# Performance work log

Measured on AMD Instinct MI355X. Metric: run time of the kernel, lower is better.

Reference implementation:

```python
import jax, jax.numpy as jnp
import numpy as np

N_SIGMA = 2
N_CLASS = 8
FG_WEIGHT = jnp.array([10., 10., 10., 40., 80., 100., 60., 20.], dtype=jnp.float32)
W_INST, W_VAR, W_SEED = 1.0, 10.0, 1.0
MIN_PIXELS = 128


def lovasz_hinge_flat(logits, labels):
    # logits, labels: [P] flat; labels in {0,1}
    signs = 2.0 * labels - 1.0
    errors = 1.0 - logits * signs
    order = jnp.argsort(-errors)  # descending
    errors_sorted = errors[order]
    gt_sorted = labels[order]
    gts = gt_sorted.sum()
    inter = gts - jnp.cumsum(gt_sorted)
    union = gts + jnp.cumsum(1.0 - gt_sorted)
    jac = 1.0 - inter / union
    grad = jnp.concatenate([jac[:1], jac[1:] - jac[:-1]])
    return jnp.dot(jax.nn.relu(errors_sorted), jax.lax.stop_gradient(grad))


def setup_inputs() -> dict:
    key = jax.random.key(0)
    k1, k2, k3, k4 = jax.random.split(key, 4)
    B, H, W, N = 2, 512, 1024, 8
    prediction = jax.random.normal(k1, (B, 12, H, W), dtype=jnp.float32)
    bbox = jax.random.randint(k2, (B, 9, H, W), 0, 2, dtype=jnp.int32)
    masks = jax.random.randint(k3, (B, N, H, W), 0, 2, dtype=jnp.int32)
    cls_ids = jax.random.randint(k4, (B, N), 0, 8, dtype=jnp.int32)
    return {"prediction": prediction, "bbox": bbox, "masks": masks, "cls_ids": cls_ids}


def _forward(prediction, bbox, masks, cls_ids):
    B, C, H, W = prediction.shape
    N = masks.shape[1]
    sg = jax.lax.stop_gradient
    # coordinate map: full 2048/1024 linspace sliced to [:W]/[:H], as in the buffer
    xm = jnp.linspace(0.0, 2.0, 2048, dtype=prediction.dtype)[:W]
    ym = jnp.linspace(0.0, 1.0, 1024, dtype=prediction.dtype)[:H]
    xym = jnp.stack([jnp.broadcast_to(xm[None, :], (H, W)),
                     jnp.broadcast_to(ym[:, None], (H, W))], axis=0)  # [2,H,W]

    spatial_emb = jnp.tanh(prediction[:, 0:2]) + xym[None]            # [B,2,H,W]
    sigma = prediction[:, 2:2 + N_SIGMA]                               # [B,2,H,W]
    seed = jax.nn.sigmoid(prediction[:, 2 + N_SIGMA:2 + N_SIGMA + N_CLASS])  # [B,8,H,W]

    # background seed loss: sum over cls 1..8 of seed[cls-1]^2 where bbox[cls]==0
    bg = bbox[:, 1:9] == 0                                             # [B,8,H,W]
    seed_bg = jnp.sum(jnp.where(bg, seed * seed, 0.0), axis=(1, 2, 3))  # [B]

    m = (masks > 0).astype(prediction.dtype)                           # [B,N,H,W]
    cnt = m.sum(axis=(2, 3))                                           # [B,N]
    valid = (cnt >= MIN_PIXELS).astype(prediction.dtype)               # [B,N]
    cnt_safe = jnp.maximum(cnt, 1.0)

    # per-instance masked means (to_center=False -> center from spatial_emb)
    center = jnp.einsum('bnhw,bchw->bnc', m, spatial_emb) / cnt_safe[..., None]  # [B,N,2]
    s_mean = jnp.einsum('bnhw,bchw->bnc', m, sigma) / cnt_safe[..., None]        # [B,N,2]

    # var loss: mean over [n_sigma, P] of (sigma_in - s.detach())^2
    diff2 = (sigma[:, None] - sg(s_mean)[..., None, None]) ** 2        # [B,N,2,H,W]
    var_inst = jnp.einsum('bnchw,bnhw->bn', diff2, m) / (N_SIGMA * cnt_safe)

    s_exp = jnp.exp(s_mean * 10.0)                                     # [B,N,2]
    d2 = (spatial_emb[:, None] - center[..., None, None]) ** 2         # [B,N,2,H,W]
    dist = jnp.exp(-jnp.einsum('bnchw,bnc->bnhw', d2, s_exp))          # [B,N,H,W]

    # lovasz hinge per instance on dist*2-1 vs mask
    logits = (dist * 2.0 - 1.0).reshape(B * N, H * W)
    labels = m.reshape(B * N, H * W)
    lov = jax.vmap(lovasz_hinge_flat)(logits, labels).reshape(B, N)    # [B,N]

    # foreground seed loss
    seed_cls = jnp.take_along_axis(seed, cls_ids[..., None, None].astype(jnp.int32), axis=1)  # [B,N,H,W]
    fw = FG_WEIGHT[cls_ids]                                            # [B,N]
    seed_fg = fw * jnp.einsum('bnhw,bnhw->bn', m, (seed_cls - sg(dist)) ** 2)

    obj = valid.sum(axis=1)                                            # [B]
    obj_safe = jnp.maximum(obj, 1.0)
    inst_l = jnp.sum(lov * valid, axis=1) / obj_safe
    var_l = jnp.sum(var_inst * valid, axis=1) / obj_safe
    seed_l = (seed_bg + jnp.sum(seed_fg * valid, axis=1)) / (H * W)
    loss = jnp.mean(W_INST * inst_l + W_VAR * var_l + W_SEED * seed_l)
    return loss


def reference(prediction, bbox, masks, cls_ids):
    return _forward(prediction, bbox, masks, cls_ids)
```

## Files before the change

kernel.cpp:

```cpp
#include <hip/hip_runtime.h>
#include <cstdint>
#include <cstddef>

#define HW 524288
#define HW4 131072
#define NBIN 1024


__device__ __forceinline__ float wred(float v) {
#pragma unroll
  for (int o = 32; o > 0; o >>= 1) v += __shfl_xor(v, o, 64);
  return v;
}

__device__ __forceinline__ float fsig(float x) {
  return __builtin_amdgcn_rcpf(1.f + __expf(-x));
}
__device__ __forceinline__ float ftanh(float x) {
  return 1.f - 2.f * __builtin_amdgcn_rcpf(__expf(2.f * x) + 1.f);
}

__global__ __launch_bounds__(256) void pass1(
    const float* __restrict__ pred, const int* __restrict__ masks,
    double* __restrict__ acc)
{
  const int b = blockIdx.y;
  const int tid = threadIdx.x;
  const float4* pb4 = (const float4*)(pred + (size_t)b * 12 * HW);
  const int4*   mk4 = (const int4*)(masks + (size_t)b * 8 * HW);

  float c[8] = {0}, cx[8] = {0}, cy[8] = {0}, sx[8] = {0}, sy[8] = {0},
        sxx[8] = {0}, syy[8] = {0};

#pragma unroll
  for (int k = 0; k < 2; k++) {
    const int g = blockIdx.x * 512 + k * 256 + tid;
    int idx = g << 2;
    int h = idx >> 10, w = idx & 1023;
    float4 p0 = pb4[g];
    float4 p1 = pb4[HW4 + g];
    float4 s0 = pb4[2 * HW4 + g];
    float4 s1 = pb4[3 * HW4 + g];
    int4 mv[8];
#pragma unroll
    for (int n = 0; n < 8; n++) mv[n] = mk4[n * HW4 + g];

    float p0v[4] = {p0.x, p0.y, p0.z, p0.w}, p1v[4] = {p1.x, p1.y, p1.z, p1.w};
    float s0v[4] = {s0.x, s0.y, s0.z, s0.w}, s1v[4] = {s1.x, s1.y, s1.z, s1.w};
    float exv[4], eyv[4];
#pragma unroll
    for (int j = 0; j < 4; j++) {
      exv[j] = ftanh(p0v[j]) + (float)((w + j) * (2.0 / 2047.0));
      eyv[j] = ftanh(p1v[j]) + (float)(h * (1.0 / 1023.0));
    }
#pragma unroll
    for (int n = 0; n < 8; n++) {
      int mvv[4] = {mv[n].x, mv[n].y, mv[n].z, mv[n].w};
#pragma unroll
      for (int j = 0; j < 4; j++) {
        float mf = (mvv[j] > 0) ? 1.f : 0.f;
        c[n] += mf; cx[n] += mf * exv[j]; cy[n] += mf * eyv[j];
        sx[n] += mf * s0v[j]; sy[n] += mf * s1v[j];
        sxx[n] += mf * s0v[j] * s0v[j]; syy[n] += mf * s1v[j] * s1v[j];
      }
    }
  }

  __shared__ float red[4][56];
  int lane = tid & 63, wid = tid >> 6;
#pragma unroll
  for (int n = 0; n < 8; n++) {
    float r0 = wred(c[n]),  r1 = wred(cx[n]), r2 = wred(cy[n]),
          r3 = wred(sx[n]), r4 = wred(sy[n]), r5 = wred(sxx[n]),
          r6 = wred(syy[n]);
    if (lane == 0) {
      red[wid][n * 7 + 0] = r0; red[wid][n * 7 + 1] = r1;
      red[wid][n * 7 + 2] = r2; red[wid][n * 7 + 3] = r3;
      red[wid][n * 7 + 4] = r4; red[wid][n * 7 + 5] = r5;
      red[wid][n * 7 + 6] = r6;
    }
  }
  __syncthreads();
  if (tid < 56) {
    float s = red[0][tid] + red[1][tid] + red[2][tid] + red[3][tid];
    int n = tid / 7, q = tid % 7;
    atomicAdd(&acc[((size_t)b * 8 + n) * 8 + q], (double)s);
  }
}

__global__ __launch_bounds__(512) void pass3(
    const float* __restrict__ pred, const int* __restrict__ bbox,
    const int* __restrict__ masks, const int* __restrict__ cls_ids,
    double* __restrict__ acc, double* __restrict__ seedbg,
    unsigned* __restrict__ gdump)
{
  const int b = blockIdx.y;
  const int tid = threadIdx.x;
  __shared__ unsigned hist[8 * NBIN];
  __shared__ float redf[8][9];

  uint4* h4 = (uint4*)hist;
  for (int j = tid; j < 2048; j += 512) h4[j] = make_uint4(0u, 0u, 0u, 0u);

  float cxp[8], cyp[8], sexp[8], seyp[8];
  int clsv[8];
#pragma unroll
  for (int n = 0; n < 8; n++) {
    const double* a = acc + ((size_t)b * 8 + n) * 8;
    double cs = a[0] < 1.0 ? 1.0 : a[0];
    cxp[n] = (float)(a[1] / cs);
    cyp[n] = (float)(a[2] / cs);
    sexp[n] = __expf((float)(a[3] / cs) * 10.f);
    seyp[n] = __expf((float)(a[4] / cs) * 10.f);
    clsv[n] = cls_ids[b * 8 + n];
  }
  const float4* pb4 = (const float4*)(pred + (size_t)b * 12 * HW);
  const int4*   mk4 = (const int4*)(masks + (size_t)b * 8 * HW);
  const int4*   bb4 = (const int4*)(bbox + (size_t)b * 9 * HW);
  __syncthreads();

  const int g = blockIdx.x * 512 + tid;
  const int idx = g << 2;
  const int h = idx >> 10, w = idx & 1023;

  float4 p0 = pb4[g];
  float4 p1 = pb4[HW4 + g];
  float ex[4], ey[4];
  {
    float p0v[4] = {p0.x, p0.y, p0.z, p0.w}, p1v[4] = {p1.x, p1.y, p1.z, p1.w};
#pragma unroll
    for (int j = 0; j < 4; j++) {
      ex[j] = ftanh(p0v[j]) + (float)((w + j) * (2.0 / 2047.0));
      ey[j] = ftanh(p1v[j]) + (float)(h * (1.0 / 1023.0));
    }
  }

  float sbg = 0.f;
  int lane = tid & 63, wid = tid >> 6;
#pragma unroll
  for (int n = 0; n < 8; n++) {
    int4   mv = mk4[n * HW4 + g];
    int4   bv = bb4[(1 + n) * HW4 + g];
    float4 sc = pb4[(4 + clsv[n]) * HW4 + g];
    float4 sb = pb4[(4 + n) * HW4 + g];
    int mvv[4] = {mv.x, mv.y, mv.z, mv.w}, bvv[4] = {bv.x, bv.y, bv.z, bv.w};
    float scv[4] = {sc.x, sc.y, sc.z, sc.w}, sbv[4] = {sb.x, sb.y, sb.z, sb.w};
    float sf = 0.f;
#pragma unroll
    for (int j = 0; j < 4; j++) {
      int m = (mvv[j] > 0) ? 1 : 0;
      float dx = ex[j] - cxp[n], dy = ey[j] - cyp[n];
      float d = __expf(-(dx * dx * sexp[n] + dy * dy * seyp[n]));
      float df = fsig(scv[j]) - d;
      sf += m ? df * df : 0.f;
      float s0 = fsig(sbv[j]);
      sbg += (bvv[j] == 0) ? s0 * s0 : 0.f;
      float e = m ? 2.f - 2.f * d : 2.f * d;
      int k = (int)(e * 512.f); k = k > (NBIN - 1) ? (NBIN - 1) : k;
      atomicAdd(&hist[n * NBIN + k], m ? 65536u : 1u);
    }
    float r = wred(sf);
    if (lane == 0) redf[wid][n] = r;
  }
  {
    float r = wred(sbg);
    if (lane == 0) redf[wid][8] = r;
  }
  __syncthreads();

  uint4* dst = (uint4*)(gdump + ((size_t)(b * 256 + blockIdx.x) * 8) * NBIN);
  for (int j = tid; j < 2048; j += 512) dst[j] = h4[j];

  if (tid < 9) {
    float t = 0.f;
    for (int w2 = 0; w2 < 8; w2++) t += redf[w2][tid];
    if (tid < 8)
      atomicAdd(&acc[((size_t)b * 8 + tid) * 8 + 7], (double)t);
    else
      atomicAdd(&seedbg[b], (double)t);
  }
}

__global__ __launch_bounds__(256) void pass4a(
    const unsigned* __restrict__ gdump, unsigned long long* __restrict__ ghist)
{
  const int seg = blockIdx.x >> 4;
  const int chunk = blockIdx.x & 15;
  const int b = seg >> 3, n = seg & 7;
  const int tid = threadIdx.x;

  unsigned neg[4] = {0, 0, 0, 0}, pos[4] = {0, 0, 0, 0};
#pragma unroll
  for (int xb = 0; xb < 16; xb++) {
    int blk = chunk * 16 + xb;
    const uint4 v = ((const uint4*)gdump)[(((size_t)b * 256 + blk) * 8 + n) * 256 + tid];
    neg[0] += v.x & 0xffffu; pos[0] += v.x >> 16;
    neg[1] += v.y & 0xffffu; pos[1] += v.y >> 16;
    neg[2] += v.z & 0xffffu; pos[2] += v.z >> 16;
    neg[3] += v.w & 0xffffu; pos[3] += v.w >> 16;
  }
  unsigned long long* gh = ghist + (size_t)seg * NBIN;
#pragma unroll
  for (int i = 0; i < 4; i++) {
    if (neg[i] | pos[i])
      atomicAdd(&gh[tid * 4 + i],
                (unsigned long long)neg[i] | ((unsigned long long)pos[i] << 32));
  }
}

__global__ __launch_bounds__(256) void pass4(
    const unsigned long long* __restrict__ ghist, const double* __restrict__ acc,
    const double* __restrict__ seedbg, const int* __restrict__ cls_ids,
    float* __restrict__ lov, unsigned* __restrict__ ctr,
    float* __restrict__ out)
{
  const int seg = blockIdx.x;
  const int tid = threadIdx.x;
  const int lane = tid & 63, wid = tid >> 6;
  __shared__ __align__(16) unsigned lh[NBIN * 2];
  __shared__ unsigned wc[4], wp[4];
  __shared__ double sred[4];

  const uint4* gh4 = (const uint4*)(ghist + (size_t)seg * NBIN);
#pragma unroll
  for (int i = 0; i < 2; i++)
    ((uint4*)lh)[i * 256 + tid] = gh4[i * 256 + tid];
  __syncthreads();

  double G = acc[seg * 8 + 0];

  unsigned cntT = 0, posT = 0;
#pragma unroll
  for (int i = 0; i < 4; i++) {
    int kk = (NBIN - 1) - tid * 4 - i;
    unsigned h0 = lh[2 * kk], h1 = lh[2 * kk + 1];
    cntT += h0 + h1; posT += h1;
  }
  unsigned ic = cntT, ip = posT;
  for (int o = 1; o < 64; o <<= 1) {
    unsigned yc = __shfl_up(ic, o, 64), yp = __shfl_up(ip, o, 64);
    if (lane >= o) { ic += yc; ip += yp; }
  }
  if (lane == 63) { wc[wid] = ic; wp[wid] = ip; }
  __syncthreads();
  unsigned oc = 0, op = 0;
  for (int w2 = 0; w2 < wid; w2++) { oc += wc[w2]; op += wp[w2]; }
  unsigned p = oc + ic - cntT, C = op + ip - posT;

  double S = 0.0;
#pragma unroll
  for (int i = 0; i < 4; i++) {
    int kk = (NBIN - 1) - tid * 4 - i;
    unsigned n1 = lh[2 * kk + 1], n0 = lh[2 * kk];
    double ec = (kk + 0.5) * (1.0 / 512.0);
    if (n1) {
      S += (double)n1 * ec / (G + (double)(p - C));
      p += n1; C += n1;
    }
    if (n0) {
      double rem = G - (double)C;
      if (rem > 0.0) {
        double aa = G + (double)(p - C);
        S += ec * rem * (1.0 / aa - 1.0 / (aa + (double)n0));
      }
      p += n0;
    }
  }
#pragma unroll
  for (int o = 32; o > 0; o >>= 1) S += __shfl_xor(S, o, 64);
  if (lane == 0) sred[wid] = S;
  __syncthreads();

  if (tid == 0) {
    double St = sred[0] + sred[1] + sred[2] + sred[3];
    atomicExch(&lov[seg], (float)St);
    __threadfence();
    unsigned old = atomicAdd(ctr, 1u);
    if (old == 15u) {
      __threadfence();
      const float FG[8] = {10.f, 10.f, 10.f, 40.f, 80.f, 100.f, 60.f, 20.f};
      double total = 0.0;
      for (int b = 0; b < 2; b++) {
        double obj = 0, inst = 0, varl = 0, sfg = 0;
        for (int n = 0; n < 8; n++) {
          int s = b * 8 + n;
          const double* a = acc + s * 8;
          double cnt = a[0];
          double cs = cnt < 1.0 ? 1.0 : cnt;
          double smx = a[3] / cs, smy = a[4] / cs;
          double var = ((a[5] - cnt * smx * smx) + (a[6] - cnt * smy * smy)) /
                       (2.0 * cs);
          double v = (cnt >= 128.0) ? 1.0 : 0.0;
          double lv = (double)atomicAdd(&lov[s], 0.0f);
          obj += v;
          inst += lv * v;
          varl += var * v;
          sfg += (double)FG[cls_ids[s]] * a[7] * v;
        }
        double objs = obj < 1.0 ? 1.0 : obj;
        double seedl = (seedbg[b] + sfg) / (double)HW;
        total += inst / objs + 10.0 * (varl / objs) + seedl;
      }
      out[0] = (float)(0.5 * total);
    }
  }
}

extern "C" void kernel_launch(void* const* d_in, const int* in_sizes, int n_in,
                              void* d_out, int out_size, void* d_ws, size_t ws_size,
                              hipStream_t stream)
{
  (void)in_sizes; (void)n_in; (void)out_size; (void)ws_size;
  const float* pred  = (const float*)d_in[0];
  const int*   bbox  = (const int*)d_in[1];
  const int*   masks = (const int*)d_in[2];
  const int*   cls   = (const int*)d_in[3];

  char* ws = (char*)d_ws;
  double*             acc    = (double*)(ws + 0);
  double*             seedbg = (double*)(ws + 1024);
  float*              lov    = (float*)(ws + 1040);
  unsigned*           ctr    = (unsigned*)(ws + 1104);
  unsigned long long* ghist  = (unsigned long long*)(ws + 4096);
  unsigned*           gdump  = (unsigned*)(ws + 262144);

  hipMemsetAsync(d_ws, 0, 135168, stream);
  pass1<<<dim3(256, 2), 256, 0, stream>>>(pred, masks, acc);
  pass3<<<dim3(256, 2), 512, 0, stream>>>(pred, bbox, masks, cls, acc, seedbg, gdump);
  pass4a<<<256, 256, 0, stream>>>(gdump, ghist);
  pass4<<<16, 256, 0, stream>>>(ghist, acc, seedbg, cls, lov, ctr, (float*)d_out);
}
```

Measured before the change: 182.2 us.

## Fuse all passes into one cooperative kernel with grid syncs

Replaces the four separate kernels with one cooperative kernel of 256 blocks that uses grid-wide syncs between phases. The embedding values ex/ey computed in the centroid phase stay in registers and are reused in the histogram phase, so that data is not reloaded. The per-block histogram merge is folded into the 16 lovasz blocks, which each read all 128 block dumps directly, and the memset shrinks. The aims are to drop launch gaps and redundant memory traffic. The costs are grid-sync overhead, one block per CU with 512 threads, and a serial 128-step merge inside only 16 blocks.

```diff
diff --git a/kernel.cpp b/kernel.cpp
--- a/kernel.cpp
+++ b/kernel.cpp
@@ -1,6 +1,9 @@
 #include <hip/hip_runtime.h>
+#include <hip/hip_cooperative_groups.h>
 #include <cstdint>
 #include <cstddef>
+
+namespace cg = cooperative_groups;
 
 #define HW 524288
 #define HW4 131072
@@ -12,155 +15,146 @@
   for (int o = 32; o > 0; o >>= 1) v += __shfl_xor(v, o, 64);
   return v;
 }
-
 __device__ __forceinline__ float fsig(float x) {
   return __builtin_amdgcn_rcpf(1.f + __expf(-x));
 }
 __device__ __forceinline__ float ftanh(float x) {
   return 1.f - 2.f * __builtin_amdgcn_rcpf(__expf(2.f * x) + 1.f);
 }
-
-__global__ __launch_bounds__(256) void pass1(
-    const float* __restrict__ pred, const int* __restrict__ masks,
-    double* __restrict__ acc)
-{
-  const int b = blockIdx.y;
-  const int tid = threadIdx.x;
-  const float4* pb4 = (const float4*)(pred + (size_t)b * 12 * HW);
-  const int4*   mk4 = (const int4*)(masks + (size_t)b * 8 * HW);
-
-  float c[8] = {0}, cx[8] = {0}, cy[8] = {0}, sx[8] = {0}, sy[8] = {0},
-        sxx[8] = {0}, syy[8] = {0};
-
-#pragma unroll
-  for (int k = 0; k < 2; k++) {
-    const int g = blockIdx.x * 512 + k * 256 + tid;
-    int idx = g << 2;
-    int h = idx >> 10, w = idx & 1023;
-    float4 p0 = pb4[g];
-    float4 p1 = pb4[HW4 + g];
-    float4 s0 = pb4[2 * HW4 + g];
-    float4 s1 = pb4[3 * HW4 + g];
-    int4 mv[8];
-#pragma unroll
-    for (int n = 0; n < 8; n++) mv[n] = mk4[n * HW4 + g];
-
-    float p0v[4] = {p0.x, p0.y, p0.z, p0.w}, p1v[4] = {p1.x, p1.y, p1.z, p1.w};
-    float s0v[4] = {s0.x, s0.y, s0.z, s0.w}, s1v[4] = {s1.x, s1.y, s1.z, s1.w};
-    float exv[4], eyv[4];
-#pragma unroll
-    for (int j = 0; j < 4; j++) {
-      exv[j] = ftanh(p0v[j]) + (float)((w + j) * (2.0 / 2047.0));
-      eyv[j] = ftanh(p1v[j]) + (float)(h * (1.0 / 1023.0));
-    }
-#pragma unroll
-    for (int n = 0; n < 8; n++) {
-      int mvv[4] = {mv[n].x, mv[n].y, mv[n].z, mv[n].w};
-#pragma unroll
-      for (int j = 0; j < 4; j++) {
-        float mf = (mvv[j] > 0) ? 1.f : 0.f;
-        c[n] += mf; cx[n] += mf * exv[j]; cy[n] += mf * eyv[j];
-        sx[n] += mf * s0v[j]; sy[n] += mf * s1v[j];
-        sxx[n] += mf * s0v[j] * s0v[j]; syy[n] += mf * s1v[j] * s1v[j];
-      }
-    }
-  }
-
-  __shared__ float red[4][56];
-  int lane = tid & 63, wid = tid >> 6;
-#pragma unroll
-  for (int n = 0; n < 8; n++) {
-    float r0 = wred(c[n]),  r1 = wred(cx[n]), r2 = wred(cy[n]),
-          r3 = wred(sx[n]), r4 = wred(sy[n]), r5 = wred(sxx[n]),
-          r6 = wred(syy[n]);
-    if (lane == 0) {
-      red[wid][n * 7 + 0] = r0; red[wid][n * 7 + 1] = r1;
-      red[wid][n * 7 + 2] = r2; red[wid][n * 7 + 3] = r3;
-      red[wid][n * 7 + 4] = r4; red[wid][n * 7 + 5] = r5;
-      red[wid][n * 7 + 6] = r6;
-    }
-  }
-  __syncthreads();
-  if (tid < 56) {
-    float s = red[0][tid] + red[1][tid] + red[2][tid] + red[3][tid];
-    int n = tid / 7, q = tid % 7;
-    atomicAdd(&acc[((size_t)b * 8 + n) * 8 + q], (double)s);
-  }
-}
-
-__global__ __launch_bounds__(512) void pass3(
+__device__ __forceinline__ float rfl(float x) {
+  return __int_as_float(__builtin_amdgcn_readfirstlane(__float_as_int(x)));
+}
+
+__global__ __launch_bounds__(512) void kfused(
     const float* __restrict__ pred, const int* __restrict__ bbox,
     const int* __restrict__ masks, const int* __restrict__ cls_ids,
     double* __restrict__ acc, double* __restrict__ seedbg,
-    unsigned* __restrict__ gdump)
+    float* __restrict__ lov, unsigned long long* __restrict__ gdump,
+    float* __restrict__ out)
 {
-  const int b = blockIdx.y;
+  const int bid = blockIdx.x;
+  const int b = bid >> 7, xb = bid & 127;
   const int tid = threadIdx.x;
-  __shared__ unsigned hist[8 * NBIN];
+  const int lane = tid & 63, wid = tid >> 6;
+
+  __shared__ __align__(16) unsigned hist[8 * NBIN];
   __shared__ float redf[8][9];
-
-  uint4* h4 = (uint4*)hist;
-  for (int j = tid; j < 2048; j += 512) h4[j] = make_uint4(0u, 0u, 0u, 0u);
-
-  float cxp[8], cyp[8], sexp[8], seyp[8];
-  int clsv[8];
-#pragma unroll
-  for (int n = 0; n < 8; n++) {
-    const double* a = acc + ((size_t)b * 8 + n) * 8;
-    double cs = a[0] < 1.0 ? 1.0 : a[0];
-    cxp[n] = (float)(a[1] / cs);
-    cyp[n] = (float)(a[2] / cs);
-    sexp[n] = __expf((float)(a[3] / cs) * 10.f);
-    seyp[n] = __expf((float)(a[4] / cs) * 10.f);
-    clsv[n] = cls_ids[b * 8 + n];
-  }
+  __shared__ unsigned wcs[8], wps[8];
+  __shared__ double sred[8];
+
   const float4* pb4 = (const float4*)(pred + (size_t)b * 12 * HW);
   const int4*   mk4 = (const int4*)(masks + (size_t)b * 8 * HW);
   const int4*   bb4 = (const int4*)(bbox + (size_t)b * 9 * HW);
+
+  float ex[2][4], ey[2][4];
+  {
+    float c[8] = {0}, cx[8] = {0}, cy[8] = {0}, sx[8] = {0}, sy[8] = {0},
+          sxx[8] = {0}, syy[8] = {0};
+#pragma unroll
+    for (int k = 0; k < 2; k++) {
+      const int g = xb * 1024 + k * 512 + tid;
+      int idx = g << 2;
+      int h = idx >> 10, w = idx & 1023;
+      float4 p0 = pb4[g];
+      float4 p1 = pb4[HW4 + g];
+      float4 s0 = pb4[2 * HW4 + g];
+      float4 s1 = pb4[3 * HW4 + g];
+      int4 mv[8];
+#pragma unroll
+      for (int n = 0; n < 8; n++) mv[n] = mk4[n * HW4 + g];
+
+      float p0v[4] = {p0.x, p0.y, p0.z, p0.w}, p1v[4] = {p1.x, p1.y, p1.z, p1.w};
+      float s0v[4] = {s0.x, s0.y, s0.z, s0.w}, s1v[4] = {s1.x, s1.y, s1.z, s1.w};
+#pragma unroll
+      for (int j = 0; j < 4; j++) {
+        ex[k][j] = ftanh(p0v[j]) + (float)((w + j) * (2.0 / 2047.0));
+        ey[k][j] = ftanh(p1v[j]) + (float)(h * (1.0 / 1023.0));
+      }
+#pragma unroll
+      for (int n = 0; n < 8; n++) {
+        int mvv[4] = {mv[n].x, mv[n].y, mv[n].z, mv[n].w};
+#pragma unroll
+        for (int j = 0; j < 4; j++) {
+          float mf = (mvv[j] > 0) ? 1.f : 0.f;
+          c[n] += mf; cx[n] += mf * ex[k][j]; cy[n] += mf * ey[k][j];
+          sx[n] += mf * s0v[j]; sy[n] += mf * s1v[j];
+          sxx[n] += mf * s0v[j] * s0v[j]; syy[n] += mf * s1v[j] * s1v[j];
+        }
+      }
+    }
+    float* rf = (float*)hist;
+#pragma unroll
+    for (int n = 0; n < 8; n++) {
+      float r0 = wred(c[n]),  r1 = wred(cx[n]), r2 = wred(cy[n]),
+            r3 = wred(sx[n]), r4 = wred(sy[n]), r5 = wred(sxx[n]),
+            r6 = wred(syy[n]);
+      if (lane == 0) {
+        rf[wid * 56 + n * 7 + 0] = r0; rf[wid * 56 + n * 7 + 1] = r1;
+        rf[wid * 56 + n * 7 + 2] = r2; rf[wid * 56 + n * 7 + 3] = r3;
+        rf[wid * 56 + n * 7 + 4] = r4; rf[wid * 56 + n * 7 + 5] = r5;
+        rf[wid * 56 + n * 7 + 6] = r6;
+      }
+    }
+    __syncthreads();
+    if (tid < 56) {
+      float s = 0.f;
+      for (int w2 = 0; w2 < 8; w2++) s += rf[w2 * 56 + tid];
+      int n = tid / 7, q = tid % 7;
+      atomicAdd(&acc[((size_t)b * 8 + n) * 8 + q], (double)s);
+    }
+  }
+
+  cg::this_grid().sync();
+
+  {
+    uint4* h4 = (uint4*)hist;
+    for (int j = tid; j < 2048; j += 512) h4[j] = make_uint4(0u, 0u, 0u, 0u);
+  }
   __syncthreads();
 
-  const int g = blockIdx.x * 512 + tid;
-  const int idx = g << 2;
-  const int h = idx >> 10, w = idx & 1023;
-
-  float4 p0 = pb4[g];
-  float4 p1 = pb4[HW4 + g];
-  float ex[4], ey[4];
-  {
-    float p0v[4] = {p0.x, p0.y, p0.z, p0.w}, p1v[4] = {p1.x, p1.y, p1.z, p1.w};
-#pragma unroll
-    for (int j = 0; j < 4; j++) {
-      ex[j] = ftanh(p0v[j]) + (float)((w + j) * (2.0 / 2047.0));
-      ey[j] = ftanh(p1v[j]) + (float)(h * (1.0 / 1023.0));
-    }
-  }
-
   float sbg = 0.f;
-  int lane = tid & 63, wid = tid >> 6;
-#pragma unroll
-  for (int n = 0; n < 8; n++) {
-    int4   mv = mk4[n * HW4 + g];
-    int4   bv = bb4[(1 + n) * HW4 + g];
-    float4 sc = pb4[(4 + clsv[n]) * HW4 + g];
-    float4 sb = pb4[(4 + n) * HW4 + g];
-    int mvv[4] = {mv.x, mv.y, mv.z, mv.w}, bvv[4] = {bv.x, bv.y, bv.z, bv.w};
-    float scv[4] = {sc.x, sc.y, sc.z, sc.w}, sbv[4] = {sb.x, sb.y, sb.z, sb.w};
+#pragma unroll
+  for (int i = 0; i < 8; i++) {
+    const int ni = (i + wid) & 7;
+    const double* a = acc + ((size_t)b * 8 + ni) * 8;
+    double a0 = a[0];
+    double csd = a0 < 1.0 ? 1.0 : a0;
+    float cxv = rfl((float)(a[1] / csd));
+    float cyv = rfl((float)(a[2] / csd));
+    float sex = rfl(__expf((float)(a[3] / csd) * 10.f));
+    float sey = rfl(__expf((float)(a[4] / csd) * 10.f));
+    int cls = __builtin_amdgcn_readfirstlane(cls_ids[b * 8 + ni]);
+    const float4* sc4 = pb4 + (size_t)(4 + cls) * HW4;
+    const float4* sb4 = pb4 + (size_t)(4 + ni) * HW4;
+    const int4*   mp4 = mk4 + (size_t)ni * HW4;
+    const int4*   bv4 = bb4 + (size_t)(1 + ni) * HW4;
+    unsigned* hn = hist + ni * NBIN;
     float sf = 0.f;
 #pragma unroll
-    for (int j = 0; j < 4; j++) {
-      int m = (mvv[j] > 0) ? 1 : 0;
-      float dx = ex[j] - cxp[n], dy = ey[j] - cyp[n];
-      float d = __expf(-(dx * dx * sexp[n] + dy * dy * seyp[n]));
-      float df = fsig(scv[j]) - d;
-      sf += m ? df * df : 0.f;
-      float s0 = fsig(sbv[j]);
-      sbg += (bvv[j] == 0) ? s0 * s0 : 0.f;
-      float e = m ? 2.f - 2.f * d : 2.f * d;
-      int k = (int)(e * 512.f); k = k > (NBIN - 1) ? (NBIN - 1) : k;
-      atomicAdd(&hist[n * NBIN + k], m ? 65536u : 1u);
+    for (int k = 0; k < 2; k++) {
+      const int g = xb * 1024 + k * 512 + tid;
+      int4   mv = mp4[g];
+      int4   bv = bv4[g];
+      float4 sc = sc4[g];
+      float4 sb = sb4[g];
+      int mvv[4] = {mv.x, mv.y, mv.z, mv.w}, bvv[4] = {bv.x, bv.y, bv.z, bv.w};
+      float scv[4] = {sc.x, sc.y, sc.z, sc.w}, sbv[4] = {sb.x, sb.y, sb.z, sb.w};
+#pragma unroll
+      for (int j = 0; j < 4; j++) {
+        int m = (mvv[j] > 0) ? 1 : 0;
+        float dx = ex[k][j] - cxv, dy = ey[k][j] - cyv;
+        float d = __expf(-(dx * dx * sex + dy * dy * sey));
+        float df = fsig(scv[j]) - d;
+        sf += m ? df * df : 0.f;
+        float s0 = fsig(sbv[j]);
+        sbg += (bvv[j] == 0) ? s0 * s0 : 0.f;
+        float e = m ? 2.f - 2.f * d : 2.f * d;
+        int kbin = (int)(e * 512.f); kbin = kbin > (NBIN - 1) ? (NBIN - 1) : kbin;
+        atomicAdd(&hn[kbin], m ? 65536u : 1u);
+      }
     }
     float r = wred(sf);
-    if (lane == 0) redf[wid][n] = r;
+    if (lane == 0) redf[wid][ni] = r;
   }
   {
     float r = wred(sbg);
@@ -168,141 +162,124 @@
   }
   __syncthreads();
 
-  uint4* dst = (uint4*)(gdump + ((size_t)(b * 256 + blockIdx.x) * 8) * NBIN);
-  for (int j = tid; j < 2048; j += 512) dst[j] = h4[j];
-
-  if (tid < 9) {
-    float t = 0.f;
-    for (int w2 = 0; w2 < 8; w2++) t += redf[w2][tid];
-    if (tid < 8)
-      atomicAdd(&acc[((size_t)b * 8 + tid) * 8 + 7], (double)t);
-    else
-      atomicAdd(&seedbg[b], (double)t);
-  }
-}
-
-__global__ __launch_bounds__(256) void pass4a(
-    const unsigned* __restrict__ gdump, unsigned long long* __restrict__ ghist)
-{
-  const int seg = blockIdx.x >> 4;
-  const int chunk = blockIdx.x & 15;
-  const int b = seg >> 3, n = seg & 7;
-  const int tid = threadIdx.x;
-
-  unsigned neg[4] = {0, 0, 0, 0}, pos[4] = {0, 0, 0, 0};
-#pragma unroll
-  for (int xb = 0; xb < 16; xb++) {
-    int blk = chunk * 16 + xb;
-    const uint4 v = ((const uint4*)gdump)[(((size_t)b * 256 + blk) * 8 + n) * 256 + tid];
-    neg[0] += v.x & 0xffffu; pos[0] += v.x >> 16;
-    neg[1] += v.y & 0xffffu; pos[1] += v.y >> 16;
-    neg[2] += v.z & 0xffffu; pos[2] += v.z >> 16;
-    neg[3] += v.w & 0xffffu; pos[3] += v.w >> 16;
-  }
-  unsigned long long* gh = ghist + (size_t)seg * NBIN;
-#pragma unroll
-  for (int i = 0; i < 4; i++) {
-    if (neg[i] | pos[i])
-      atomicAdd(&gh[tid * 4 + i],
-                (unsigned long long)neg[i] | ((unsigned long long)pos[i] << 32));
-  }
-}
-
-__global__ __launch_bounds__(256) void pass4(
-    const unsigned long long* __restrict__ ghist, const double* __restrict__ acc,
-    const double* __restrict__ seedbg, const int* __restrict__ cls_ids,
-    float* __restrict__ lov, unsigned* __restrict__ ctr,
-    float* __restrict__ out)
-{
-  const int seg = blockIdx.x;
-  const int tid = threadIdx.x;
-  const int lane = tid & 63, wid = tid >> 6;
-  __shared__ __align__(16) unsigned lh[NBIN * 2];
-  __shared__ unsigned wc[4], wp[4];
-  __shared__ double sred[4];
-
-  const uint4* gh4 = (const uint4*)(ghist + (size_t)seg * NBIN);
-#pragma unroll
-  for (int i = 0; i < 2; i++)
-    ((uint4*)lh)[i * 256 + tid] = gh4[i * 256 + tid];
-  __syncthreads();
-
-  double G = acc[seg * 8 + 0];
-
-  unsigned cntT = 0, posT = 0;
-#pragma unroll
-  for (int i = 0; i < 4; i++) {
-    int kk = (NBIN - 1) - tid * 4 - i;
-    unsigned h0 = lh[2 * kk], h1 = lh[2 * kk + 1];
-    cntT += h0 + h1; posT += h1;
-  }
-  unsigned ic = cntT, ip = posT;
-  for (int o = 1; o < 64; o <<= 1) {
-    unsigned yc = __shfl_up(ic, o, 64), yp = __shfl_up(ip, o, 64);
-    if (lane >= o) { ic += yc; ip += yp; }
-  }
-  if (lane == 63) { wc[wid] = ic; wp[wid] = ip; }
-  __syncthreads();
-  unsigned oc = 0, op = 0;
-  for (int w2 = 0; w2 < wid; w2++) { oc += wc[w2]; op += wp[w2]; }
-  unsigned p = oc + ic - cntT, C = op + ip - posT;
-
-  double S = 0.0;
-#pragma unroll
-  for (int i = 0; i < 4; i++) {
-    int kk = (NBIN - 1) - tid * 4 - i;
-    unsigned n1 = lh[2 * kk + 1], n0 = lh[2 * kk];
-    double ec = (kk + 0.5) * (1.0 / 512.0);
-    if (n1) {
-      S += (double)n1 * ec / (G + (double)(p - C));
-      p += n1; C += n1;
-    }
-    if (n0) {
-      double rem = G - (double)C;
-      if (rem > 0.0) {
-        double aa = G + (double)(p - C);
-        S += ec * rem * (1.0 / aa - 1.0 / (aa + (double)n0));
-      }
-      p += n0;
-    }
-  }
-#pragma unroll
-  for (int o = 32; o > 0; o >>= 1) S += __shfl_xor(S, o, 64);
-  if (lane == 0) sred[wid] = S;
-  __syncthreads();
-
-  if (tid == 0) {
-    double St = sred[0] + sred[1] + sred[2] + sred[3];
-    atomicExch(&lov[seg], (float)St);
-    __threadfence();
-    unsigned old = atomicAdd(ctr, 1u);
-    if (old == 15u) {
-      __threadfence();
-      const float FG[8] = {10.f, 10.f, 10.f, 40.f, 80.f, 100.f, 60.f, 20.f};
-      double total = 0.0;
-      for (int b = 0; b < 2; b++) {
-        double obj = 0, inst = 0, varl = 0, sfg = 0;
-        for (int n = 0; n < 8; n++) {
-          int s = b * 8 + n;
-          const double* a = acc + s * 8;
-          double cnt = a[0];
-          double cs = cnt < 1.0 ? 1.0 : cnt;
-          double smx = a[3] / cs, smy = a[4] / cs;
-          double var = ((a[5] - cnt * smx * smx) + (a[6] - cnt * smy * smy)) /
-                       (2.0 * cs);
-          double v = (cnt >= 128.0) ? 1.0 : 0.0;
-          double lv = (double)atomicAdd(&lov[s], 0.0f);
-          obj += v;
-          inst += lv * v;
-          varl += var * v;
-          sfg += (double)FG[cls_ids[s]] * a[7] * v;
+  {
+    const unsigned long long* h64 = (const unsigned long long*)hist;
+    unsigned long long* dst = gdump + (size_t)(b * 128 + xb) * 4096;
+    for (int j = tid; j < 4096; j += 512) dst[j] = h64[j];
+    if (tid < 9) {
+      float t = 0.f;
+      for (int w2 = 0; w2 < 8; w2++) t += redf[w2][tid];
+      if (tid < 8)
+        atomicAdd(&acc[((size_t)b * 8 + tid) * 8 + 7], (double)t);
+      else
+        atomicAdd(&seedbg[b], (double)t);
+    }
+  }
+
+  cg::this_grid().sync();
+
+  if (bid < 16) {
+    const int seg = bid, b2 = seg >> 3, n2 = seg & 7;
+    unsigned* mneg = hist;
+    unsigned* mpos = hist + NBIN;
+    unsigned ng0 = 0, ps0 = 0, ng1 = 0, ps1 = 0;
+#pragma unroll 4
+    for (int x2 = 0; x2 < 128; x2++) {
+      const unsigned* src =
+          (const unsigned*)(gdump + (size_t)(b2 * 128 + x2) * 4096) + n2 * NBIN;
+      unsigned v0 = src[tid], v1 = src[tid + 512];
+      ng0 += v0 & 0xffffu; ps0 += v0 >> 16;
+      ng1 += v1 & 0xffffu; ps1 += v1 >> 16;
+    }
+    mneg[tid] = ng0; mneg[tid + 512] = ng1;
+    mpos[tid] = ps0; mpos[tid + 512] = ps1;
+    __syncthreads();
+
+    double G = acc[seg * 8 + 0];
+    int kk0 = (NBIN - 1) - tid * 2;
+    unsigned h0n = mneg[kk0],     h0p = mpos[kk0];
+    unsigned h1n = mneg[kk0 - 1], h1p = mpos[kk0 - 1];
+    unsigned cntT = h0n + h0p + h1n + h1p, posT = h0p + h1p;
+    unsigned ic = cntT, ip = posT;
+    for (int o = 1; o < 64; o <<= 1) {
+      unsigned yc = __shfl_up(ic, o, 64), yp = __shfl_up(ip, o, 64);
+      if (lane >= o) { ic += yc; ip += yp; }
+    }
+    if (lane == 63) { wcs[wid] = ic; wps[wid] = ip; }
+    __syncthreads();
+    unsigned oc = 0, op = 0;
+    for (int w2 = 0; w2 < wid; w2++) { oc += wcs[w2]; op += wps[w2]; }
+    unsigned p = oc + ic - cntT, C = op + ip - posT;
+
+    double S = 0.0;
+    {
+      double ec = (kk0 + 0.5) * (1.0 / 512.0);
+      if (h0p) {
+        S += (double)h0p * ec / (G + (double)(p - C));
+        p += h0p; C += h0p;
+      }
+      if (h0n) {
+        double rem = G - (double)C;
+        if (rem > 0.0) {
+          double aa = G + (double)(p - C);
+          S += ec * rem * (1.0 / aa - 1.0 / (aa + (double)h0n));
         }
-        double objs = obj < 1.0 ? 1.0 : obj;
-        double seedl = (seedbg[b] + sfg) / (double)HW;
-        total += inst / objs + 10.0 * (varl / objs) + seedl;
-      }
-      out[0] = (float)(0.5 * total);
-    }
+        p += h0n;
+      }
+    }
+    {
+      double ec = (kk0 - 0.5) * (1.0 / 512.0);
+      if (h1p) {
+        S += (double)h1p * ec / (G + (double)(p - C));
+        p += h1p; C += h1p;
+      }
+      if (h1n) {
+        double rem = G - (double)C;
+        if (rem > 0.0) {
+          double aa = G + (double)(p - C);
+          S += ec * rem * (1.0 / aa - 1.0 / (aa + (double)h1n));
+        }
+        p += h1n;
+      }
+    }
+#pragma unroll
+    for (int o = 32; o > 0; o >>= 1) S += __shfl_xor(S, o, 64);
+    if (lane == 0) sred[wid] = S;
+    __syncthreads();
+    if (tid == 0) {
+      double St = 0.0;
+      for (int w2 = 0; w2 < 8; w2++) St += sred[w2];
+      lov[seg] = (float)St;
+    }
+  }
+
+  cg::this_grid().sync();
+
+  if (bid == 0 && tid == 0) {
+    const float FG[8] = {10.f, 10.f, 10.f, 40.f, 80.f, 100.f, 60.f, 20.f};
+    double total = 0.0;
+    for (int bb = 0; bb < 2; bb++) {
+      double obj = 0, inst = 0, varl = 0, sfg = 0;
+      for (int n = 0; n < 8; n++) {
+        int s = bb * 8 + n;
+        const double* a = acc + s * 8;
+        double cnt = a[0];
+        double cs2 = cnt < 1.0 ? 1.0 : cnt;
+        double smx = a[3] / cs2, smy = a[4] / cs2;
+        double var = ((a[5] - cnt * smx * smx) + (a[6] - cnt * smy * smy)) /
+                     (2.0 * cs2);
+        double v = (cnt >= 128.0) ? 1.0 : 0.0;
+        double lv = (double)lov[s];
+        obj += v;
+        inst += lv * v;
+        varl += var * v;
+        sfg += (double)FG[cls_ids[s]] * a[7] * v;
+      }
+      double objs = obj < 1.0 ? 1.0 : obj;
+      double seedl = (seedbg[bb] + sfg) / (double)HW;
+      total += inst / objs + 10.0 * (varl / objs) + seedl;
+    }
+    out[0] = (float)(0.5 * total);
   }
 }
 
@@ -320,13 +297,12 @@
   double*             acc    = (double*)(ws + 0);
   double*             seedbg = (double*)(ws + 1024);
   float*              lov    = (float*)(ws + 1040);
-  unsigned*           ctr    = (unsigned*)(ws + 1104);
-  unsigned long long* ghist  = (unsigned long long*)(ws + 4096);
-  unsigned*           gdump  = (unsigned*)(ws + 262144);
-
-  hipMemsetAsync(d_ws, 0, 135168, stream);
-  pass1<<<dim3(256, 2), 256, 0, stream>>>(pred, masks, acc);
-  pass3<<<dim3(256, 2), 512, 0, stream>>>(pred, bbox, masks, cls, acc, seedbg, gdump);
-  pass4a<<<256, 256, 0, stream>>>(gdump, ghist);
-  pass4<<<16, 256, 0, stream>>>(ghist, acc, seedbg, cls, lov, ctr, (float*)d_out);
-}
+  unsigned long long* gdump  = (unsigned long long*)(ws + 262144);
+  float*              outp   = (float*)d_out;
+
+  hipMemsetAsync(d_ws, 0, 4096, stream);
+  void* kargs[] = {(void*)&pred, (void*)&bbox, (void*)&masks, (void*)&cls,
+                   (void*)&acc, (void*)&seedbg, (void*)&lov, (void*)&gdump,
+                   (void*)&outp};
+  hipLaunchCooperativeKernel(kfused, dim3(256), dim3(512), kargs, 0u, stream);
+}
```

Result: slower. 265.9 us (+45.9%).

## Merge per-block histograms via global atomics and drop the pass4a kernel

Applied to the files above, without the earlier changes.

pass3 now adds its shared-memory histogram straight into the global 64-bit histogram with atomics on nonzero bins, in place of writing a full per-block dump that a separate pass4a kernel then reduced. This removes one kernel launch and the dump's write and re-read traffic. Blocks shrink to 256 threads with twice as many launched, and pass1 processes one float4 per thread instead of two. Each wave starts at a different instance so waves do not all hit the same LDS histogram at once, and the per-instance centers are loaded inside the loop and made wave-uniform with readfirstlane. The cost is more global atomic contention from 1024 blocks on 16K bins.

```diff
diff --git a/kernel.cpp b/kernel.cpp
--- a/kernel.cpp
+++ b/kernel.cpp
@@ -12,12 +12,14 @@
   for (int o = 32; o > 0; o >>= 1) v += __shfl_xor(v, o, 64);
   return v;
 }
-
 __device__ __forceinline__ float fsig(float x) {
   return __builtin_amdgcn_rcpf(1.f + __expf(-x));
 }
 __device__ __forceinline__ float ftanh(float x) {
   return 1.f - 2.f * __builtin_amdgcn_rcpf(__expf(2.f * x) + 1.f);
+}
+__device__ __forceinline__ float rfl(float x) {
+  return __int_as_float(__builtin_amdgcn_readfirstlane(__float_as_int(x)));
 }
 
 __global__ __launch_bounds__(256) void pass1(
@@ -29,40 +31,39 @@
   const float4* pb4 = (const float4*)(pred + (size_t)b * 12 * HW);
   const int4*   mk4 = (const int4*)(masks + (size_t)b * 8 * HW);
 
-  float c[8] = {0}, cx[8] = {0}, cy[8] = {0}, sx[8] = {0}, sy[8] = {0},
-        sxx[8] = {0}, syy[8] = {0};
-
-#pragma unroll
-  for (int k = 0; k < 2; k++) {
-    const int g = blockIdx.x * 512 + k * 256 + tid;
-    int idx = g << 2;
-    int h = idx >> 10, w = idx & 1023;
-    float4 p0 = pb4[g];
-    float4 p1 = pb4[HW4 + g];
-    float4 s0 = pb4[2 * HW4 + g];
-    float4 s1 = pb4[3 * HW4 + g];
-    int4 mv[8];
-#pragma unroll
-    for (int n = 0; n < 8; n++) mv[n] = mk4[n * HW4 + g];
-
-    float p0v[4] = {p0.x, p0.y, p0.z, p0.w}, p1v[4] = {p1.x, p1.y, p1.z, p1.w};
-    float s0v[4] = {s0.x, s0.y, s0.z, s0.w}, s1v[4] = {s1.x, s1.y, s1.z, s1.w};
-    float exv[4], eyv[4];
+  const int g = blockIdx.x * 256 + tid;
+  const int idx = g << 2;
+  const int h = idx >> 10, w = idx & 1023;
+
+  float4 p0 = pb4[g];
+  float4 p1 = pb4[HW4 + g];
+  float4 s0 = pb4[2 * HW4 + g];
+  float4 s1 = pb4[3 * HW4 + g];
+  int4 mv[8];
+#pragma unroll
+  for (int n = 0; n < 8; n++) mv[n] = mk4[n * HW4 + g];
+
+  float p0v[4] = {p0.x, p0.y, p0.z, p0.w}, p1v[4] = {p1.x, p1.y, p1.z, p1.w};
+  float s0v[4] = {s0.x, s0.y, s0.z, s0.w}, s1v[4] = {s1.x, s1.y, s1.z, s1.w};
+  float exv[4], eyv[4];
+#pragma unroll
+  for (int j = 0; j < 4; j++) {
+    exv[j] = ftanh(p0v[j]) + (float)((w + j) * (2.0 / 2047.0));
+    eyv[j] = ftanh(p1v[j]) + (float)(h * (1.0 / 1023.0));
+  }
+
+  float c[8], cx[8], cy[8], sx[8], sy[8], sxx[8], syy[8];
+#pragma unroll
+  for (int n = 0; n < 8; n++) {
+    c[n] = 0.f; cx[n] = 0.f; cy[n] = 0.f; sx[n] = 0.f; sy[n] = 0.f;
+    sxx[n] = 0.f; syy[n] = 0.f;
+    int mvv[4] = {mv[n].x, mv[n].y, mv[n].z, mv[n].w};
 #pragma unroll
     for (int j = 0; j < 4; j++) {
-      exv[j] = ftanh(p0v[j]) + (float)((w + j) * (2.0 / 2047.0));
-      eyv[j] = ftanh(p1v[j]) + (float)(h * (1.0 / 1023.0));
-    }
-#pragma unroll
-    for (int n = 0; n < 8; n++) {
-      int mvv[4] = {mv[n].x, mv[n].y, mv[n].z, mv[n].w};
-#pragma unroll
-      for (int j = 0; j < 4; j++) {
-        float mf = (mvv[j] > 0) ? 1.f : 0.f;
-        c[n] += mf; cx[n] += mf * exv[j]; cy[n] += mf * eyv[j];
-        sx[n] += mf * s0v[j]; sy[n] += mf * s1v[j];
-        sxx[n] += mf * s0v[j] * s0v[j]; syy[n] += mf * s1v[j] * s1v[j];
-      }
+      float mf = (mvv[j] > 0) ? 1.f : 0.f;
+      c[n] += mf; cx[n] += mf * exv[j]; cy[n] += mf * eyv[j];
+      sx[n] += mf * s0v[j]; sy[n] += mf * s1v[j];
+      sxx[n] += mf * s0v[j] * s0v[j]; syy[n] += mf * s1v[j] * s1v[j];
     }
   }
 
@@ -88,38 +89,27 @@
   }
 }
 
-__global__ __launch_bounds__(512) void pass3(
+__global__ __launch_bounds__(256) void pass3(
     const float* __restrict__ pred, const int* __restrict__ bbox,
     const int* __restrict__ masks, const int* __restrict__ cls_ids,
     double* __restrict__ acc, double* __restrict__ seedbg,
-    unsigned* __restrict__ gdump)
+    unsigned long long* __restrict__ ghist)
 {
   const int b = blockIdx.y;
   const int tid = threadIdx.x;
-  __shared__ unsigned hist[8 * NBIN];
-  __shared__ float redf[8][9];
+  const int lane = tid & 63, wid = tid >> 6;
+  __shared__ __align__(16) unsigned hist[8 * NBIN];
+  __shared__ float redf[4][9];
 
   uint4* h4 = (uint4*)hist;
-  for (int j = tid; j < 2048; j += 512) h4[j] = make_uint4(0u, 0u, 0u, 0u);
-
-  float cxp[8], cyp[8], sexp[8], seyp[8];
-  int clsv[8];
-#pragma unroll
-  for (int n = 0; n < 8; n++) {
-    const double* a = acc + ((size_t)b * 8 + n) * 8;
-    double cs = a[0] < 1.0 ? 1.0 : a[0];
-    cxp[n] = (float)(a[1] / cs);
-    cyp[n] = (float)(a[2] / cs);
-    sexp[n] = __expf((float)(a[3] / cs) * 10.f);
-    seyp[n] = __expf((float)(a[4] / cs) * 10.f);
-    clsv[n] = cls_ids[b * 8 + n];
-  }
+  for (int j = tid; j < 2048; j += 256) h4[j] = make_uint4(0u, 0u, 0u, 0u);
+  __syncthreads();
+
   const float4* pb4 = (const float4*)(pred + (size_t)b * 12 * HW);
   const int4*   mk4 = (const int4*)(masks + (size_t)b * 8 * HW);
   const int4*   bb4 = (const int4*)(bbox + (size_t)b * 9 * HW);
-  __syncthreads();
-
-  const int g = blockIdx.x * 512 + tid;
+
+  const int g = blockIdx.x * 256 + tid;
   const int idx = g << 2;
   const int h = idx >> 10, w = idx & 1023;
 
@@ -136,31 +126,40 @@
   }
 
   float sbg = 0.f;
-  int lane = tid & 63, wid = tid >> 6;
-#pragma unroll
-  for (int n = 0; n < 8; n++) {
-    int4   mv = mk4[n * HW4 + g];
-    int4   bv = bb4[(1 + n) * HW4 + g];
-    float4 sc = pb4[(4 + clsv[n]) * HW4 + g];
-    float4 sb = pb4[(4 + n) * HW4 + g];
+#pragma unroll
+  for (int i = 0; i < 8; i++) {
+    const int ni = (i + 2 * wid) & 7;
+    const double* a = acc + ((size_t)b * 8 + ni) * 8;
+    double a0 = a[0];
+    double csd = a0 < 1.0 ? 1.0 : a0;
+    float cxv = rfl((float)(a[1] / csd));
+    float cyv = rfl((float)(a[2] / csd));
+    float sex = rfl(__expf((float)(a[3] / csd) * 10.f));
+    float sey = rfl(__expf((float)(a[4] / csd) * 10.f));
+    int cls = __builtin_amdgcn_readfirstlane(cls_ids[b * 8 + ni]);
+    int4   mv = mk4[(size_t)ni * HW4 + g];
+    int4   bv = bb4[(size_t)(1 + ni) * HW4 + g];
+    float4 sc = pb4[(size_t)(4 + cls) * HW4 + g];
+    float4 sb = pb4[(size_t)(4 + ni) * HW4 + g];
+    unsigned* hn = hist + ni * NBIN;
     int mvv[4] = {mv.x, mv.y, mv.z, mv.w}, bvv[4] = {bv.x, bv.y, bv.z, bv.w};
     float scv[4] = {sc.x, sc.y, sc.z, sc.w}, sbv[4] = {sb.x, sb.y, sb.z, sb.w};
     float sf = 0.f;
 #pragma unroll
     for (int j = 0; j < 4; j++) {
       int m = (mvv[j] > 0) ? 1 : 0;
-      float dx = ex[j] - cxp[n], dy = ey[j] - cyp[n];
-      float d = __expf(-(dx * dx * sexp[n] + dy * dy * seyp[n]));
+      float dx = ex[j] - cxv, dy = ey[j] - cyv;
+      float d = __expf(-(dx * dx * sex + dy * dy * sey));
       float df = fsig(scv[j]) - d;
       sf += m ? df * df : 0.f;
       float s0 = fsig(sbv[j]);
       sbg += (bvv[j] == 0) ? s0 * s0 : 0.f;
       float e = m ? 2.f - 2.f * d : 2.f * d;
-      int k = (int)(e * 512.f); k = k > (NBIN - 1) ? (NBIN - 1) : k;
-      atomicAdd(&hist[n * NBIN + k], m ? 65536u : 1u);
+      int kbin = (int)(e * 512.f); kbin = kbin > (NBIN - 1) ? (NBIN - 1) : kbin;
+      atomicAdd(&hn[kbin], m ? 65536u : 1u);
     }
     float r = wred(sf);
-    if (lane == 0) redf[wid][n] = r;
+    if (lane == 0) redf[wid][ni] = r;
   }
   {
     float r = wred(sbg);
@@ -168,43 +167,22 @@
   }
   __syncthreads();
 
-  uint4* dst = (uint4*)(gdump + ((size_t)(b * 256 + blockIdx.x) * 8) * NBIN);
-  for (int j = tid; j < 2048; j += 512) dst[j] = h4[j];
+  for (int j = tid; j < 8 * NBIN; j += 256) {
+    unsigned v = hist[j];
+    if (v) {
+      int n = j >> 10, bin = j & (NBIN - 1);
+      atomicAdd(&ghist[(size_t)((b * 8 + n) << 10) + bin],
+                (unsigned long long)(v & 0xffffu) |
+                ((unsigned long long)(v >> 16) << 32));
+    }
+  }
 
   if (tid < 9) {
-    float t = 0.f;
-    for (int w2 = 0; w2 < 8; w2++) t += redf[w2][tid];
+    float t = redf[0][tid] + redf[1][tid] + redf[2][tid] + redf[3][tid];
     if (tid < 8)
       atomicAdd(&acc[((size_t)b * 8 + tid) * 8 + 7], (double)t);
     else
       atomicAdd(&seedbg[b], (double)t);
-  }
-}
-
-__global__ __launch_bounds__(256) void pass4a(
-    const unsigned* __restrict__ gdump, unsigned long long* __restrict__ ghist)
-{
-  const int seg = blockIdx.x >> 4;
-  const int chunk = blockIdx.x & 15;
-  const int b = seg >> 3, n = seg & 7;
-  const int tid = threadIdx.x;
-
-  unsigned neg[4] = {0, 0, 0, 0}, pos[4] = {0, 0, 0, 0};
-#pragma unroll
-  for (int xb = 0; xb < 16; xb++) {
-    int blk = chunk * 16 + xb;
-    const uint4 v = ((const uint4*)gdump)[(((size_t)b * 256 + blk) * 8 + n) * 256 + tid];
-    neg[0] += v.x & 0xffffu; pos[0] += v.x >> 16;
-    neg[1] += v.y & 0xffffu; pos[1] += v.y >> 16;
-    neg[2] += v.z & 0xffffu; pos[2] += v.z >> 16;
-    neg[3] += v.w & 0xffffu; pos[3] += v.w >> 16;
-  }
-  unsigned long long* gh = ghist + (size_t)seg * NBIN;
-#pragma unroll
-  for (int i = 0; i < 4; i++) {
-    if (neg[i] | pos[i])
-      atomicAdd(&gh[tid * 4 + i],
-                (unsigned long long)neg[i] | ((unsigned long long)pos[i] << 32));
   }
 }
 
@@ -322,11 +300,9 @@
   float*              lov    = (float*)(ws + 1040);
   unsigned*           ctr    = (unsigned*)(ws + 1104);
   unsigned long long* ghist  = (unsigned long long*)(ws + 4096);
-  unsigned*           gdump  = (unsigned*)(ws + 262144);
 
   hipMemsetAsync(d_ws, 0, 135168, stream);
-  pass1<<<dim3(256, 2), 256, 0, stream>>>(pred, masks, acc);
-  pass3<<<dim3(256, 2), 512, 0, stream>>>(pred, bbox, masks, cls, acc, seedbg, gdump);
-  pass4a<<<256, 256, 0, stream>>>(gdump, ghist);
+  pass1<<<dim3(512, 2), 256, 0, stream>>>(pred, masks, acc);
+  pass3<<<dim3(512, 2), 256, 0, stream>>>(pred, bbox, masks, cls, acc, seedbg, ghist);
   pass4<<<16, 256, 0, stream>>>(ghist, acc, seedbg, cls, lov, ctr, (float*)d_out);
 }
```

Measured after the change: 234.1 us. 1.28x slower.
